# Kernel tuning notes

Hardware: AMD Instinct MI355X
Metric: run time of the kernel (lower is better)

The kernel has to match this reference:

```python
import jax, jax.numpy as jnp
import numpy as np

D_MODEL = 1024
NUM_HEADS = 16
D_K = D_MODEL // NUM_HEADS
B, S = 2, 2048
NEG = -1e9


def setup_inputs() -> dict:
    key = jax.random.key(0)
    ks = jax.random.split(key, 12)
    sc = 1.0 / np.sqrt(D_MODEL)
    inp = {
        'Q': jax.random.normal(ks[0], (B, S, D_MODEL), jnp.float32),
        'K': jax.random.normal(ks[1], (B, S, D_MODEL), jnp.float32),
        'V': jax.random.normal(ks[2], (B, S, D_MODEL), jnp.float32),
        # causal additive mask: 1.0 above diagonal -> scores += mask * -1e9
        'mask': jnp.triu(jnp.ones((S, S), jnp.float32), k=1),
        'Wq': jax.random.normal(ks[3], (D_MODEL, D_MODEL), jnp.float32) * sc,
        'bq': jnp.zeros((D_MODEL,), jnp.float32),
        'Wk': jax.random.normal(ks[4], (D_MODEL, D_MODEL), jnp.float32) * sc,
        'bk': jnp.zeros((D_MODEL,), jnp.float32),
        'Wv': jax.random.normal(ks[5], (D_MODEL, D_MODEL), jnp.float32) * sc,
        'bv': jnp.zeros((D_MODEL,), jnp.float32),
        'Wo': jax.random.normal(ks[6], (D_MODEL, D_MODEL), jnp.float32) * sc,
        'bo': jnp.zeros((D_MODEL,), jnp.float32),
    }
    return inp


def _split_heads(x):
    # [B,S,D] -> [B,H,S,d_k]
    b, s, _ = x.shape
    return x.reshape(b, s, NUM_HEADS, D_K).transpose(0, 2, 1, 3)


def reference(Q, K, V, mask, Wq, bq, Wk, bk, Wv, bv, Wo, bo):
    # torch Linear: y = x @ W.T + b
    q = _split_heads(Q @ Wq.T + bq)  # [B,H,S,d_k]
    k = _split_heads(K @ Wk.T + bk)
    v = _split_heads(V @ Wv.T + bv)
    scores = jnp.einsum('bhqd,bhkd->bhqk', q, k) / np.sqrt(D_K)
    scores = scores + mask * NEG  # mask broadcasts over [B,H]
    probs = jax.nn.softmax(scores, axis=-1)
    attn = jnp.einsum('bhqk,bhkd->bhqd', probs, v)  # [B,H,S,d_k]
    attn = attn.transpose(0, 2, 1, 3).reshape(Q.shape[0], Q.shape[1], D_MODEL)
    return attn @ Wo.T + bo
```

## Files before the change

kernel.cpp:

```cpp
#include <hip/hip_runtime.h>
#include <cstdint>
#include <cstddef>

#define D_MODEL 1024
#define NHEADS  16
#define DK      64
#define BATCH   2
#define SEQ     2048
#define MTOT    (BATCH*SEQ)

typedef unsigned short u16;
typedef __attribute__((ext_vector_type(8))) __bf16 bf16x8;
typedef __attribute__((ext_vector_type(4))) float  f32x4;
typedef __attribute__((ext_vector_type(4))) uint32_t u32x4;

#define QSCALE 0.18033688f

static __device__ __forceinline__ void gload16(const void* g, void* l) {
  __builtin_amdgcn_global_load_lds((const __attribute__((address_space(1))) void*)g,
                                   (__attribute__((address_space(3))) void*)l,
                                   16, 0, 0);
}

static __device__ __forceinline__ float bfu(u16 x) {
  union { uint32_t u; float f; } v; v.u = (uint32_t)x << 16; return v.f;
}

__global__ void cast_all_kernel(
    const float* __restrict__ Q, const float* __restrict__ K, const float* __restrict__ V,
    const float* __restrict__ Wq, const float* __restrict__ Wk,
    const float* __restrict__ Wv, const float* __restrict__ Wo,
    u16* __restrict__ dstX, u16* __restrict__ dstW) {
  constexpr int NX = MTOT * D_MODEL;
  constexpr int NW = D_MODEL * D_MODEL;
  const int i = (blockIdx.x * blockDim.x + threadIdx.x) * 4;
  const float* src;
  u16* dst;
  if (i < 3 * NX) {
    dst = dstX + i;
    src = (i < NX) ? Q + i : (i < 2 * NX) ? K + (i - NX) : V + (i - 2 * NX);
  } else {
    const int j = i - 3 * NX;
    dst = dstW + j;
    const int ws = j >> 20;
    const int jo = j & (NW - 1);
    src = (ws == 0) ? Wq + jo : (ws == 1) ? Wk + jo : (ws == 2) ? Wv + jo : Wo + jo;
  }
  float4 f = *reinterpret_cast<const float4*>(src);
  union { __bf16 h[4]; ushort4 s; } o;
  o.h[0] = (__bf16)f.x; o.h[1] = (__bf16)f.y; o.h[2] = (__bf16)f.z; o.h[3] = (__bf16)f.w;
  *reinterpret_cast<ushort4*>(dst) = o.s;
}

__global__ __launch_bounds__(256, 3) void gemm_qkv(
    const u16* __restrict__ A,
    const u16* __restrict__ W0, const u16* __restrict__ W1, const u16* __restrict__ W2,
    const float* __restrict__ b0, const float* __restrict__ b1, const float* __restrict__ b2,
    u16* __restrict__ out_q, u16* __restrict__ out_k, u16* __restrict__ out_v) {
  constexpr int K = 1024;
  constexpr int EP = 136;
  __shared__ __align__(16) u16 smem[128 * EP];
  u16* lA = smem;
  u16* lB = smem + 128 * 64;
  const int w = threadIdx.x >> 6, lane = threadIdx.x & 63;
  const int blockM = blockIdx.x * 128, blockN = blockIdx.y * 128;
  const int sel = blockIdx.x >> 5;
  const u16*  Bt   = sel == 0 ? W0 : (sel == 1 ? W1 : W2);
  const float* bias = sel == 0 ? b0 : (sel == 1 ? b1 : b2);
  const int wm = (w >> 1) * 64, wn = (w & 1) * 64;
  f32x4 acc[4][4] = {};
  for (int kt = 0; kt < K; kt += 64) {
#pragma unroll
    for (int it = 0; it < 4; ++it) {
      int rowb = w * 32 + it * 8;
      int row  = rowb + (lane >> 3);
      int cc   = (lane & 7) * 8;
      gload16(A  + (size_t)(blockM + row) * K + kt + cc, &lA[rowb * 64]);
      gload16(Bt + (size_t)(blockN + row) * K + kt + cc, &lB[rowb * 64]);
    }
    __syncthreads();
#pragma unroll
    for (int kc = 0; kc < 2; ++kc) {
      bf16x8 af[4], bfr[4];
#pragma unroll
      for (int i = 0; i < 4; ++i)
        af[i] = *(const bf16x8*)&lA[(wm + i * 16 + (lane & 15)) * 64 + kc * 32 + (lane >> 4) * 8];
#pragma unroll
      for (int j = 0; j < 4; ++j)
        bfr[j] = *(const bf16x8*)&lB[(wn + j * 16 + (lane & 15)) * 64 + kc * 32 + (lane >> 4) * 8];
#pragma unroll
      for (int i = 0; i < 4; ++i)
#pragma unroll
        for (int j = 0; j < 4; ++j)
          acc[i][j] = __builtin_amdgcn_mfma_f32_16x16x32_bf16(af[i], bfr[j], acc[i][j], 0, 0, 0);
    }
    __syncthreads();
  }
  if (sel == 2) {
#pragma unroll
    for (int i = 0; i < 4; ++i)
#pragma unroll
      for (int j = 0; j < 4; ++j) {
        int m0 = blockM + wm + i * 16 + (lane >> 4) * 4;
        int n  = blockN + wn + j * 16 + (lane & 15);
        int ml = m0 & (MTOT - 1);
        int b = ml >> 11, s = ml & (SEQ - 1), h = n >> 6, d = n & (DK - 1);
        union { __bf16 h4[4]; ushort4 s4; } st;
#pragma unroll
        for (int r = 0; r < 4; ++r) st.h4[r] = (__bf16)(acc[i][j][r] + bias[n]);
        *(ushort4*)&out_v[(((size_t)(b * NHEADS + h)) * DK + d) * SEQ + s] = st.s4;
      }
  } else {
#pragma unroll
    for (int i = 0; i < 4; ++i)
#pragma unroll
      for (int j = 0; j < 4; ++j) {
        int n = blockN + wn + j * 16 + (lane & 15);
        float bn = bias[n];
#pragma unroll
        for (int r = 0; r < 4; ++r) {
          float val = acc[i][j][r] + bn;
          if (sel == 0) val *= QSCALE;
          union { __bf16 h2; u16 u; } cv; cv.h2 = (__bf16)val;
          smem[(wm + i * 16 + (lane >> 4) * 4 + r) * EP + wn + j * 16 + (lane & 15)] = cv.u;
        }
      }
    __syncthreads();
    u16* outqk = sel ? out_k : out_q;
    const int t = threadIdx.x;
    const int seg = t & 15;
    const int h = (blockN >> 6) + (seg >> 3);
    const int d = (seg & 7) * 8;
#pragma unroll
    for (int pass = 0; pass < 8; ++pass) {
      const int row = pass * 16 + (t >> 4);
      u32x4 vdat = *(const u32x4*)&smem[row * EP + seg * 8];
      const int m = blockM + row;
      const int ml = m & (MTOT - 1);
      const int b = ml >> 11, s = ml & (SEQ - 1);
      *(u32x4*)&outqk[(((size_t)(b * NHEADS + h)) * SEQ + s) * DK + d] = vdat;
    }
  }
}

__global__ __launch_bounds__(256, 2) void gemm_out(
    const u16* __restrict__ A, const u16* __restrict__ Bt,
    const float* __restrict__ bias, float* __restrict__ outp) {
  constexpr int K = 1024, N = 1024;
  __shared__ __align__(16) u16 lA[64 * 64];
  __shared__ __align__(16) u16 lB[128 * 64];
  const int w = threadIdx.x >> 6, lane = threadIdx.x & 63;
  const int blockM = blockIdx.x * 64, blockN = blockIdx.y * 128;
  const int wm = (w >> 1) * 32, wn = (w & 1) * 64;
  f32x4 acc[2][4] = {};
  for (int kt = 0; kt < K; kt += 64) {
#pragma unroll
    for (int it = 0; it < 2; ++it) {
      int rowb = w * 16 + it * 8;
      int row  = rowb + (lane >> 3);
      int cc   = (lane & 7) * 8;
      gload16(A + (size_t)(blockM + row) * K + kt + cc, &lA[rowb * 64]);
    }
#pragma unroll
    for (int it = 0; it < 4; ++it) {
      int rowb = w * 32 + it * 8;
      int row  = rowb + (lane >> 3);
      int cc   = (lane & 7) * 8;
      gload16(Bt + (size_t)(blockN + row) * K + kt + cc, &lB[rowb * 64]);
    }
    __syncthreads();
#pragma unroll
    for (int kc = 0; kc < 2; ++kc) {
      bf16x8 af[2], bfr[4];
#pragma unroll
      for (int i = 0; i < 2; ++i)
        af[i] = *(const bf16x8*)&lA[(wm + i * 16 + (lane & 15)) * 64 + kc * 32 + (lane >> 4) * 8];
#pragma unroll
      for (int j = 0; j < 4; ++j)
        bfr[j] = *(const bf16x8*)&lB[(wn + j * 16 + (lane & 15)) * 64 + kc * 32 + (lane >> 4) * 8];
#pragma unroll
      for (int i = 0; i < 2; ++i)
#pragma unroll
        for (int j = 0; j < 4; ++j)
          acc[i][j] = __builtin_amdgcn_mfma_f32_16x16x32_bf16(af[i], bfr[j], acc[i][j], 0, 0, 0);
    }
    __syncthreads();
  }
#pragma unroll
  for (int i = 0; i < 2; ++i)
#pragma unroll
    for (int j = 0; j < 4; ++j)
#pragma unroll
      for (int r = 0; r < 4; ++r) {
        int m = blockM + wm + i * 16 + (lane >> 4) * 4 + r;
        int n = blockN + wn + j * 16 + (lane & 15);
        outp[(size_t)m * N + n] = acc[i][j][r] + bias[n];
      }
}

static __device__ __forceinline__ void stage_kv8(
    const u16* kp, const u16* vp, int j0,
    u16* bufK, u16* bufV, int w, int lane) {
  const int rsub = lane >> 3;
  const int cl = ((lane & 7) ^ rsub) << 3;
  const int rowb = w * 8;
  gload16(kp + (size_t)(j0 + rowb + rsub) * DK + cl, bufK + rowb * 64);
  gload16(vp + (size_t)(rowb + rsub) * SEQ + j0 + cl, bufV + rowb * 64);
}

__global__ __launch_bounds__(512, 4) void attn_kernel(
    const u16* __restrict__ qh, const u16* __restrict__ kh,
    const u16* __restrict__ vt, u16* __restrict__ attnb,
    u16* __restrict__ pO, float2* __restrict__ pML) {
  __shared__ __align__(16) u16 lKV[2][2][64 * 64];
  const int w = threadIdx.x >> 6, lane = threadIdx.x & 63;
  const int g = lane >> 4, q15 = lane & 15;
  const int lid = blockIdx.x;
  const int xcd = lid & 7;
  const int idx = lid >> 3;
  const int p   = idx & 3;
  const int sraw = idx >> 2;
  const int s = 39 - sraw;
  const int bh = xcd * 4 + p;
  int qt, c, nch;
  if (s < 4)       { qt = s;                 c = 0;          nch = 1; }
  else if (s < 12) { int u = s - 4;  qt = 4 + (u >> 1); c = u & 1;  nch = 2; }
  else if (s < 24) { int u = s - 12; int q3 = u / 3; qt = 8 + q3; c = u - q3 * 3; nch = 3; }
  else             { int u = s - 24; qt = 12 + (u >> 2); c = u & 3; nch = 4; }
  const int nt_full = 2 * qt + 2;
  const int t_begin = c * 8;
  const int t_end   = min(t_begin + 8, nt_full);
  const int split   = nch > 1;
  const int b = bh >> 4, h = bh & 15;
  const u16* qp = qh + (size_t)bh * SEQ * DK;
  const u16* kp = kh + (size_t)bh * SEQ * DK;
  const u16* vp = vt + (size_t)bh * DK * SEQ;

  const int qbase = qt * 128;
  const int qrow = qbase + w * 16 + q15;
  const int wave_max_row = qbase + w * 16 + 15;
  bf16x8 aq[2];
  const u16* qr = qp + (size_t)qrow * DK;
#pragma unroll
  for (int kc = 0; kc < 2; ++kc)
    aq[kc] = *(const bf16x8*)(qr + kc * 32 + g * 8);

  float m_run = -1e30f, l_run = 0.f;
  f32x4 oacc[4] = {};
  stage_kv8(kp, vp, t_begin * 64, lKV[t_begin & 1][0], lKV[t_begin & 1][1], w, lane);

  for (int t = t_begin; t < t_end; ++t) {
    __syncthreads();
    const int cur = t & 1;
    if (t + 1 < t_end)
      stage_kv8(kp, vp, (t + 1) * 64, lKV[cur ^ 1][0], lKV[cur ^ 1][1], w, lane);
    if (64 * t > wave_max_row) continue;
    const u16* bK = lKV[cur][0];
    const u16* bV = lKV[cur][1];

    f32x4 sacc[4] = {};
    __builtin_amdgcn_s_setprio(1);
#pragma unroll
    for (int kc = 0; kc < 2; ++kc)
#pragma unroll
      for (int nb = 0; nb < 4; ++nb) {
        const int rr = nb * 16 + q15;
        const int cc = kc * 4 + g;
        bf16x8 kf = *(const bf16x8*)&bK[rr * 64 + ((cc ^ (rr & 7)) << 3)];
        sacc[nb] = __builtin_amdgcn_mfma_f32_16x16x32_bf16(kf, aq[kc], sacc[nb], 0, 0, 0);
      }
    __builtin_amdgcn_s_setprio(0);

    float pvv[4][4];
    float mx = -1e30f;
    const bool dg = (64 * t + 63) > (qbase + w * 16);
    if (dg) {
#pragma unroll
      for (int nb = 0; nb < 4; ++nb)
#pragma unroll
        for (int r = 0; r < 4; ++r) {
          float ss = sacc[nb][r];
          if (t * 64 + nb * 16 + g * 4 + r > qrow) ss = -1e30f;
          pvv[nb][r] = ss;
          mx = fmaxf(mx, ss);
        }
    } else {
#pragma unroll
      for (int nb = 0; nb < 4; ++nb)
#pragma unroll
        for (int r = 0; r < 4; ++r) {
          float ss = sacc[nb][r];
          pvv[nb][r] = ss;
          mx = fmaxf(mx, ss);
        }
    }
    mx = fmaxf(mx, __shfl_xor(mx, 16));
    mx = fmaxf(mx, __shfl_xor(mx, 32));
    if (__any(mx > m_run + 8.0f)) {
      const float mn = fmaxf(m_run, mx);
      const float alpha = __builtin_amdgcn_exp2f(m_run - mn);
      m_run = mn;
      l_run *= alpha;
#pragma unroll
      for (int nd = 0; nd < 4; ++nd)
#pragma unroll
        for (int r = 0; r < 4; ++r) oacc[nd][r] *= alpha;
    }
    float rs = 0.f;
#pragma unroll
    for (int nb = 0; nb < 4; ++nb)
#pragma unroll
      for (int r = 0; r < 4; ++r) {
        float e = __builtin_amdgcn_exp2f(pvv[nb][r] - m_run);
        pvv[nb][r] = e;
        rs += e;
      }
    rs += __shfl_xor(rs, 16);
    rs += __shfl_xor(rs, 32);
    l_run += rs;

    uint32_t pk[4][2];
#pragma unroll
    for (int nb = 0; nb < 4; ++nb) {
      union { __bf16 h2[2]; uint32_t u; } t0, t1;
      t0.h2[0] = (__bf16)pvv[nb][0]; t0.h2[1] = (__bf16)pvv[nb][1];
      t1.h2[0] = (__bf16)pvv[nb][2]; t1.h2[1] = (__bf16)pvv[nb][3];
      pk[nb][0] = t0.u; pk[nb][1] = t1.u;
    }

#pragma unroll
    for (int jc = 0; jc < 2; ++jc) {
      union { u32x4 u; bf16x8 bvec; } pf;
      const int sgbase = (g & 1) * 2;
#pragma unroll
      for (int W = 0; W < 4; ++W) {
        const int src = (sgbase + (W >> 1)) * 16 + q15;
        const uint32_t lo = (uint32_t)__shfl((int)pk[2 * jc][W & 1], src, 64);
        const uint32_t hi = (uint32_t)__shfl((int)pk[2 * jc + 1][W & 1], src, 64);
        pf.u[W] = (lane >= 32) ? hi : lo;
      }
      __builtin_amdgcn_s_setprio(1);
#pragma unroll
      for (int nd = 0; nd < 4; ++nd) {
        const int rr = nd * 16 + q15;
        const int cc = jc * 4 + g;
        bf16x8 vf = *(const bf16x8*)&bV[rr * 64 + ((cc ^ (rr & 7)) << 3)];
        oacc[nd] = __builtin_amdgcn_mfma_f32_16x16x32_bf16(vf, pf.bvec, oacc[nd], 0, 0, 0);
      }
      __builtin_amdgcn_s_setprio(0);
    }
  }

  if (!split) {
    const float rl = 1.0f / l_run;
#pragma unroll
    for (int nd = 0; nd < 4; ++nd) {
      union { __bf16 h4[4]; ushort4 s4; } st;
      st.h4[0] = (__bf16)(oacc[nd][0] * rl);
      st.h4[1] = (__bf16)(oacc[nd][1] * rl);
      st.h4[2] = (__bf16)(oacc[nd][2] * rl);
      st.h4[3] = (__bf16)(oacc[nd][3] * rl);
      *(ushort4*)&attnb[((size_t)(b * SEQ + qrow)) * D_MODEL + h * 64 + nd * 16 + g * 4] = st.s4;
    }
  } else {
    const int pid = bh * 36 + (s - 4);
    u16* po = pO + (size_t)pid * 8192 + (w * 16 + q15) * 64;
#pragma unroll
    for (int nd = 0; nd < 4; ++nd) {
      union { __bf16 h4[4]; ushort4 s4; } st;
      st.h4[0] = (__bf16)oacc[nd][0];
      st.h4[1] = (__bf16)oacc[nd][1];
      st.h4[2] = (__bf16)oacc[nd][2];
      st.h4[3] = (__bf16)oacc[nd][3];
      *(ushort4*)(po + nd * 16 + g * 4) = st.s4;
    }
    if (g == 0) {
      float2 ml; ml.x = m_run; ml.y = l_run;
      pML[(size_t)pid * 128 + w * 16 + q15] = ml;
    }
  }
}

__global__ __launch_bounds__(256) void attn_combine(
    const u16* __restrict__ pO, const float2* __restrict__ pML,
    u16* __restrict__ attnb) {
  const int blk = blockIdx.x;
  const int bh = blk / 12, qi = blk - (blk / 12) * 12;
  const int qt = 4 + qi;
  const int b = bh >> 4, h = bh & 15;
  int nch, sbase;
  if (qt < 8)       { nch = 2; sbase = 4 + (qt - 4) * 2; }
  else if (qt < 12) { nch = 3; sbase = 12 + (qt - 8) * 3; }
  else              { nch = 4; sbase = 24 + (qt - 12) * 4; }
  const int pbase = bh * 36 + (sbase - 4);
  const int t = threadIdx.x;
  const int c0 = (t & 3) * 16;

#pragma unroll
  for (int rp = 0; rp < 2; ++rp) {
    const int row = rp * 64 + (t >> 2);
    float m[4] = {-1e30f, -1e30f, -1e30f, -1e30f};
    float l[4] = {0.f, 0.f, 0.f, 0.f};
    float M = -1e30f;
#pragma unroll
    for (int i = 0; i < 4; ++i)
      if (i < nch) {
        float2 ml = pML[(size_t)(pbase + i) * 128 + row];
        m[i] = ml.x; l[i] = ml.y;
        M = fmaxf(M, ml.x);
      }
    float denom = 0.f, sc[4];
#pragma unroll
    for (int i = 0; i < 4; ++i) {
      sc[i] = __builtin_amdgcn_exp2f(m[i] - M);
      denom += l[i] * sc[i];
    }
    const float inv = 1.0f / denom;
    float out[16] = {};
#pragma unroll
    for (int i = 0; i < 4; ++i)
      if (i < nch) {
        const float scale = sc[i] * inv;
        const u16* pp = pO + (size_t)(pbase + i) * 8192 + row * 64 + c0;
        u32x4 d0 = *(const u32x4*)pp;
        u32x4 d1 = *(const u32x4*)(pp + 8);
#pragma unroll
        for (int k = 0; k < 4; ++k) {
          out[2 * k + 0] += scale * bfu((u16)(d0[k] & 0xffffu));
          out[2 * k + 1] += scale * bfu((u16)(d0[k] >> 16));
          out[8 + 2 * k + 0] += scale * bfu((u16)(d1[k] & 0xffffu));
          out[8 + 2 * k + 1] += scale * bfu((u16)(d1[k] >> 16));
        }
      }
    union { __bf16 h8[8]; u32x4 s; } o0, o1;
#pragma unroll
    for (int k = 0; k < 8; ++k) { o0.h8[k] = (__bf16)out[k]; o1.h8[k] = (__bf16)out[8 + k]; }
    u16* dst = attnb + ((size_t)(b * SEQ + qt * 128 + row)) * D_MODEL + h * 64 + c0;
    *(u32x4*)dst = o0.s;
    *(u32x4*)(dst + 8) = o1.s;
  }
}

extern "C" void kernel_launch(void* const* d_in, const int* in_sizes, int n_in,
                              void* d_out, int out_size, void* d_ws, size_t ws_size,
                              hipStream_t stream) {
  (void)in_sizes; (void)n_in; (void)out_size; (void)ws_size;
  const float* Q  = (const float*)d_in[0];
  const float* K  = (const float*)d_in[1];
  const float* V  = (const float*)d_in[2];
  const float* Wq = (const float*)d_in[4];
  const float* bq = (const float*)d_in[5];
  const float* Wk = (const float*)d_in[6];
  const float* bk = (const float*)d_in[7];
  const float* Wv = (const float*)d_in[8];
  const float* bv = (const float*)d_in[9];
  const float* Wo = (const float*)d_in[10];
  const float* bo = (const float*)d_in[11];

  char* ws = (char*)d_ws;
  size_t off = 0;
  auto carve = [&](size_t bytes) { char* p = ws + off; off += bytes; return p; };
  const size_t szX = (size_t)MTOT * D_MODEL * 2;
  const size_t szW = (size_t)D_MODEL * D_MODEL * 2;
  u16* Qb  = (u16*)carve(szX);
  u16* Kb  = (u16*)carve(szX);
  u16* Vb  = (u16*)carve(szX);
  u16* Wqb = (u16*)carve(szW);
  u16* Wkb = (u16*)carve(szW);
  u16* Wvb = (u16*)carve(szW);
  u16* Wob = (u16*)carve(szW);
  u16* qhB = (u16*)carve(szX);
  u16* khB = (u16*)carve(szX);
  u16* vtB = (u16*)carve(szX);
  u16* attnb = Qb;
  u16*    pO  = (u16*)Kb;
  float2* pML = (float2*)((char*)Kb + (size_t)19 * 1024 * 1024);
  (void)Wkb; (void)Wvb;

  const int nTot = 3 * MTOT * D_MODEL + 4 * D_MODEL * D_MODEL;
  cast_all_kernel<<<nTot / 1024, 256, 0, stream>>>(Q, K, V, Wq, Wk, Wv, Wo, Qb, Wqb);

  gemm_qkv<<<dim3(3 * MTOT / 128, D_MODEL / 128), 256, 0, stream>>>(
      Qb, Wqb, Wkb, Wvb, bq, bk, bv, qhB, khB, vtB);

  attn_kernel<<<1280, 512, 0, stream>>>(qhB, khB, vtB, attnb, pO, pML);

  attn_combine<<<384, 256, 0, stream>>>(pO, pML, attnb);

  gemm_out<<<dim3(MTOT / 64, D_MODEL / 128), 256, 0, stream>>>(attnb, Wob, bo, (float*)d_out);
}
```

Before: 124.3 us.

## Switch attention kernel to 32x32x16 MFMA with 4 waves of 32 query rows

Reworks the attention kernel so each wave handles 32 query rows using 32x32x16 bf16 MFMA instead of 16x16x32, cutting the block from 8 to 4 waves (256 threads). The P-matrix register shuffle is simplified to a single xor-32 exchange, and K/V staging now issues two loads per thread. The aim is fewer MFMA issues, fewer cross-lane shuffles and larger per-wave tiles. The trade-offs are higher register pressure per wave, fewer waves per block to hide latency, and coarser causal-skip granularity on diagonal tiles.

```diff
diff --git a/kernel.cpp b/kernel.cpp
--- a/kernel.cpp
+++ b/kernel.cpp
@@ -12,6 +12,7 @@
 typedef unsigned short u16;
 typedef __attribute__((ext_vector_type(8))) __bf16 bf16x8;
 typedef __attribute__((ext_vector_type(4))) float  f32x4;
+typedef __attribute__((ext_vector_type(16))) float f32x16;
 typedef __attribute__((ext_vector_type(4))) uint32_t u32x4;
 
 #define QSCALE 0.18033688f
@@ -198,23 +199,26 @@
       }
 }
 
-static __device__ __forceinline__ void stage_kv8(
+static __device__ __forceinline__ void stage_kv(
     const u16* kp, const u16* vp, int j0,
     u16* bufK, u16* bufV, int w, int lane) {
   const int rsub = lane >> 3;
   const int cl = ((lane & 7) ^ rsub) << 3;
-  const int rowb = w * 8;
-  gload16(kp + (size_t)(j0 + rowb + rsub) * DK + cl, bufK + rowb * 64);
-  gload16(vp + (size_t)(rowb + rsub) * SEQ + j0 + cl, bufV + rowb * 64);
-}
-
-__global__ __launch_bounds__(512, 4) void attn_kernel(
+#pragma unroll
+  for (int it = 0; it < 2; ++it) {
+    const int rowb = w * 16 + it * 8;
+    gload16(kp + (size_t)(j0 + rowb + rsub) * DK + cl, bufK + rowb * 64);
+    gload16(vp + (size_t)(rowb + rsub) * SEQ + j0 + cl, bufV + rowb * 64);
+  }
+}
+
+__global__ __launch_bounds__(256) void attn_kernel(
     const u16* __restrict__ qh, const u16* __restrict__ kh,
     const u16* __restrict__ vt, u16* __restrict__ attnb,
     u16* __restrict__ pO, float2* __restrict__ pML) {
   __shared__ __align__(16) u16 lKV[2][2][64 * 64];
   const int w = threadIdx.x >> 6, lane = threadIdx.x & 63;
-  const int g = lane >> 4, q15 = lane & 15;
+  const int q31 = lane & 31, h = lane >> 5;
   const int lid = blockIdx.x;
   const int xcd = lid & 7;
   const int idx = lid >> 3;
@@ -231,70 +235,65 @@
   const int t_begin = c * 8;
   const int t_end   = min(t_begin + 8, nt_full);
   const int split   = nch > 1;
-  const int b = bh >> 4, h = bh & 15;
+  const int b = bh >> 4, hd = bh & 15;
   const u16* qp = qh + (size_t)bh * SEQ * DK;
   const u16* kp = kh + (size_t)bh * SEQ * DK;
   const u16* vp = vt + (size_t)bh * DK * SEQ;
 
   const int qbase = qt * 128;
-  const int qrow = qbase + w * 16 + q15;
-  const int wave_max_row = qbase + w * 16 + 15;
-  bf16x8 aq[2];
+  const int qrow = qbase + w * 32 + q31;
+  const int wave_max_row = qbase + w * 32 + 31;
+  bf16x8 aq[4];
   const u16* qr = qp + (size_t)qrow * DK;
 #pragma unroll
-  for (int kc = 0; kc < 2; ++kc)
-    aq[kc] = *(const bf16x8*)(qr + kc * 32 + g * 8);
+  for (int kc = 0; kc < 4; ++kc)
+    aq[kc] = *(const bf16x8*)(qr + kc * 16 + h * 8);
 
   float m_run = -1e30f, l_run = 0.f;
-  f32x4 oacc[4] = {};
-  stage_kv8(kp, vp, t_begin * 64, lKV[t_begin & 1][0], lKV[t_begin & 1][1], w, lane);
+  f32x16 oacc[2] = {};
+  stage_kv(kp, vp, t_begin * 64, lKV[t_begin & 1][0], lKV[t_begin & 1][1], w, lane);
 
   for (int t = t_begin; t < t_end; ++t) {
     __syncthreads();
     const int cur = t & 1;
     if (t + 1 < t_end)
-      stage_kv8(kp, vp, (t + 1) * 64, lKV[cur ^ 1][0], lKV[cur ^ 1][1], w, lane);
+      stage_kv(kp, vp, (t + 1) * 64, lKV[cur ^ 1][0], lKV[cur ^ 1][1], w, lane);
     if (64 * t > wave_max_row) continue;
     const u16* bK = lKV[cur][0];
     const u16* bV = lKV[cur][1];
 
-    f32x4 sacc[4] = {};
+    f32x16 sacc[2] = {};
     __builtin_amdgcn_s_setprio(1);
 #pragma unroll
-    for (int kc = 0; kc < 2; ++kc)
-#pragma unroll
-      for (int nb = 0; nb < 4; ++nb) {
-        const int rr = nb * 16 + q15;
-        const int cc = kc * 4 + g;
+    for (int kc = 0; kc < 4; ++kc)
+#pragma unroll
+      for (int jb = 0; jb < 2; ++jb) {
+        const int rr = jb * 32 + q31;
+        const int cc = kc * 2 + h;
         bf16x8 kf = *(const bf16x8*)&bK[rr * 64 + ((cc ^ (rr & 7)) << 3)];
-        sacc[nb] = __builtin_amdgcn_mfma_f32_16x16x32_bf16(kf, aq[kc], sacc[nb], 0, 0, 0);
+        sacc[jb] = __builtin_amdgcn_mfma_f32_32x32x16_bf16(kf, aq[kc], sacc[jb], 0, 0, 0);
       }
     __builtin_amdgcn_s_setprio(0);
 
-    float pvv[4][4];
     float mx = -1e30f;
-    const bool dg = (64 * t + 63) > (qbase + w * 16);
+    const bool dg = (64 * t + 63) > (qbase + w * 32);
     if (dg) {
 #pragma unroll
-      for (int nb = 0; nb < 4; ++nb)
-#pragma unroll
-        for (int r = 0; r < 4; ++r) {
-          float ss = sacc[nb][r];
-          if (t * 64 + nb * 16 + g * 4 + r > qrow) ss = -1e30f;
-          pvv[nb][r] = ss;
+      for (int jb = 0; jb < 2; ++jb)
+#pragma unroll
+        for (int r = 0; r < 16; ++r) {
+          float ss = sacc[jb][r];
+          const int j = t * 64 + jb * 32 + (r & 3) + 8 * (r >> 2) + 4 * h;
+          if (j > qrow) ss = -1e30f;
+          sacc[jb][r] = ss;
           mx = fmaxf(mx, ss);
         }
     } else {
 #pragma unroll
-      for (int nb = 0; nb < 4; ++nb)
-#pragma unroll
-        for (int r = 0; r < 4; ++r) {
-          float ss = sacc[nb][r];
-          pvv[nb][r] = ss;
-          mx = fmaxf(mx, ss);
-        }
-    }
-    mx = fmaxf(mx, __shfl_xor(mx, 16));
+      for (int jb = 0; jb < 2; ++jb)
+#pragma unroll
+        for (int r = 0; r < 16; ++r) mx = fmaxf(mx, sacc[jb][r]);
+    }
     mx = fmaxf(mx, __shfl_xor(mx, 32));
     if (__any(mx > m_run + 8.0f)) {
       const float mn = fmaxf(m_run, mx);
@@ -302,50 +301,57 @@
       m_run = mn;
       l_run *= alpha;
 #pragma unroll
-      for (int nd = 0; nd < 4; ++nd)
-#pragma unroll
-        for (int r = 0; r < 4; ++r) oacc[nd][r] *= alpha;
+      for (int db = 0; db < 2; ++db)
+#pragma unroll
+        for (int r = 0; r < 16; ++r) oacc[db][r] *= alpha;
     }
     float rs = 0.f;
 #pragma unroll
-    for (int nb = 0; nb < 4; ++nb)
-#pragma unroll
-      for (int r = 0; r < 4; ++r) {
-        float e = __builtin_amdgcn_exp2f(pvv[nb][r] - m_run);
-        pvv[nb][r] = e;
+    for (int jb = 0; jb < 2; ++jb)
+#pragma unroll
+      for (int r = 0; r < 16; ++r) {
+        float e = __builtin_amdgcn_exp2f(sacc[jb][r] - m_run);
+        sacc[jb][r] = e;
         rs += e;
       }
-    rs += __shfl_xor(rs, 16);
     rs += __shfl_xor(rs, 32);
     l_run += rs;
 
-    uint32_t pk[4][2];
-#pragma unroll
-    for (int nb = 0; nb < 4; ++nb) {
-      union { __bf16 h2[2]; uint32_t u; } t0, t1;
-      t0.h2[0] = (__bf16)pvv[nb][0]; t0.h2[1] = (__bf16)pvv[nb][1];
-      t1.h2[0] = (__bf16)pvv[nb][2]; t1.h2[1] = (__bf16)pvv[nb][3];
-      pk[nb][0] = t0.u; pk[nb][1] = t1.u;
-    }
-
-#pragma unroll
-    for (int jc = 0; jc < 2; ++jc) {
+    uint32_t pk[2][4][2];
+#pragma unroll
+    for (int jb = 0; jb < 2; ++jb)
+#pragma unroll
+      for (int G = 0; G < 4; ++G)
+#pragma unroll
+        for (int u = 0; u < 2; ++u) {
+          union { __bf16 h2[2]; uint32_t v; } cv;
+          cv.h2[0] = (__bf16)sacc[jb][4 * G + 2 * u];
+          cv.h2[1] = (__bf16)sacc[jb][4 * G + 2 * u + 1];
+          pk[jb][G][u] = cv.v;
+        }
+
+#pragma unroll
+    for (int jseg = 0; jseg < 4; ++jseg) {
+      const int jb = jseg >> 1;
+      const int G0 = (jseg & 1) * 2;
+      const uint32_t s0 = h ? pk[jb][G0 + 1][0] : pk[jb][G0][0];
+      const uint32_t s1 = h ? pk[jb][G0 + 1][1] : pk[jb][G0][1];
+      const uint32_t e0 = h ? pk[jb][G0][0] : pk[jb][G0 + 1][0];
+      const uint32_t e1 = h ? pk[jb][G0][1] : pk[jb][G0 + 1][1];
+      const uint32_t f0 = (uint32_t)__shfl_xor((int)e0, 32);
+      const uint32_t f1 = (uint32_t)__shfl_xor((int)e1, 32);
       union { u32x4 u; bf16x8 bvec; } pf;
-      const int sgbase = (g & 1) * 2;
-#pragma unroll
-      for (int W = 0; W < 4; ++W) {
-        const int src = (sgbase + (W >> 1)) * 16 + q15;
-        const uint32_t lo = (uint32_t)__shfl((int)pk[2 * jc][W & 1], src, 64);
-        const uint32_t hi = (uint32_t)__shfl((int)pk[2 * jc + 1][W & 1], src, 64);
-        pf.u[W] = (lane >= 32) ? hi : lo;
-      }
+      pf.u[0] = h ? f0 : s0;
+      pf.u[1] = h ? f1 : s1;
+      pf.u[2] = h ? s0 : f0;
+      pf.u[3] = h ? s1 : f1;
       __builtin_amdgcn_s_setprio(1);
 #pragma unroll
-      for (int nd = 0; nd < 4; ++nd) {
-        const int rr = nd * 16 + q15;
-        const int cc = jc * 4 + g;
+      for (int db = 0; db < 2; ++db) {
+        const int rr = db * 32 + q31;
+        const int cc = jseg * 2 + h;
         bf16x8 vf = *(const bf16x8*)&bV[rr * 64 + ((cc ^ (rr & 7)) << 3)];
-        oacc[nd] = __builtin_amdgcn_mfma_f32_16x16x32_bf16(vf, pf.bvec, oacc[nd], 0, 0, 0);
+        oacc[db] = __builtin_amdgcn_mfma_f32_32x32x16_bf16(vf, pf.bvec, oacc[db], 0, 0, 0);
       }
       __builtin_amdgcn_s_setprio(0);
     }
@@ -354,29 +360,29 @@
   if (!split) {
     const float rl = 1.0f / l_run;
 #pragma unroll
-    for (int nd = 0; nd < 4; ++nd) {
-      union { __bf16 h4[4]; ushort4 s4; } st;
-      st.h4[0] = (__bf16)(oacc[nd][0] * rl);
-      st.h4[1] = (__bf16)(oacc[nd][1] * rl);
-      st.h4[2] = (__bf16)(oacc[nd][2] * rl);
-      st.h4[3] = (__bf16)(oacc[nd][3] * rl);
-      *(ushort4*)&attnb[((size_t)(b * SEQ + qrow)) * D_MODEL + h * 64 + nd * 16 + g * 4] = st.s4;
-    }
+    for (int db = 0; db < 2; ++db)
+#pragma unroll
+      for (int G = 0; G < 4; ++G) {
+        union { __bf16 h4[4]; ushort4 s4; } st;
+#pragma unroll
+        for (int e = 0; e < 4; ++e) st.h4[e] = (__bf16)(oacc[db][4 * G + e] * rl);
+        *(ushort4*)&attnb[((size_t)(b * SEQ + qrow)) * D_MODEL + hd * 64 + db * 32 + 8 * G + 4 * h] = st.s4;
+      }
   } else {
     const int pid = bh * 36 + (s - 4);
-    u16* po = pO + (size_t)pid * 8192 + (w * 16 + q15) * 64;
-#pragma unroll
-    for (int nd = 0; nd < 4; ++nd) {
-      union { __bf16 h4[4]; ushort4 s4; } st;
-      st.h4[0] = (__bf16)oacc[nd][0];
-      st.h4[1] = (__bf16)oacc[nd][1];
-      st.h4[2] = (__bf16)oacc[nd][2];
-      st.h4[3] = (__bf16)oacc[nd][3];
-      *(ushort4*)(po + nd * 16 + g * 4) = st.s4;
-    }
-    if (g == 0) {
+    u16* po = pO + (size_t)pid * 8192 + (size_t)(w * 32 + q31) * 64;
+#pragma unroll
+    for (int db = 0; db < 2; ++db)
+#pragma unroll
+      for (int G = 0; G < 4; ++G) {
+        union { __bf16 h4[4]; ushort4 s4; } st;
+#pragma unroll
+        for (int e = 0; e < 4; ++e) st.h4[e] = (__bf16)oacc[db][4 * G + e];
+        *(ushort4*)(po + db * 32 + 8 * G + 4 * h) = st.s4;
+      }
+    if (h == 0) {
       float2 ml; ml.x = m_run; ml.y = l_run;
-      pML[(size_t)pid * 128 + w * 16 + q15] = ml;
+      pML[(size_t)pid * 128 + w * 32 + q31] = ml;
     }
   }
 }
@@ -483,7 +489,7 @@
   gemm_qkv<<<dim3(3 * MTOT / 128, D_MODEL / 128), 256, 0, stream>>>(
       Qb, Wqb, Wkb, Wvb, bq, bk, bv, qhB, khB, vtB);
 
-  attn_kernel<<<1280, 512, 0, stream>>>(qhB, khB, vtB, attnb, pO, pML);
+  attn_kernel<<<1280, 256, 0, stream>>>(qhB, khB, vtB, attnb, pO, pML);
 
   attn_combine<<<384, 256, 0, stream>>>(pO, pML, attnb);
 
```

Result: no change. 124.3 us (+0.0%).
